# Optimization experiments

Measured on AMD Instinct MI355X. Metric: run time of the kernel, lower is better.

## Reference

```python
import jax, jax.numpy as jnp
import numpy as np

N_HEAD = 16
HEAD_SIZE = 64
N_EMBD = 1024
B, T = 4, 2048
THETA = 10000.0


def _rope_cos_sin(t_len, dim):
    # freqs: (dim//2,), angles: (T, dim//2)
    inv = 1.0 / (THETA ** (jnp.arange(0, dim, 2, dtype=jnp.float32) / dim))
    ang = jnp.arange(t_len, dtype=jnp.float32)[:, None] * inv[None, :]
    return jnp.cos(ang), jnp.sin(ang)


def _apply_rope(x, cos, sin):
    # x: (B, H, T, hs) -> complex-pair rotation over last dim
    xr = x.reshape(*x.shape[:-1], -1, 2)
    x0, x1 = xr[..., 0], xr[..., 1]
    c = cos[None, None, :, :]
    s = sin[None, None, :, :]
    o0 = x0 * c - x1 * s
    o1 = x0 * s + x1 * c
    return jnp.stack([o0, o1], axis=-1).reshape(x.shape)


def setup_inputs() -> dict:
    key = jax.random.key(0)
    ks = jax.random.split(key, 5)
    scale = 1.0 / np.sqrt(N_EMBD)
    return {
        "x": jax.random.normal(ks[0], (B, T, N_EMBD), dtype=jnp.float32),
        "Wq": jax.random.normal(ks[1], (N_EMBD, N_HEAD * HEAD_SIZE), dtype=jnp.float32) * scale,
        "Wk": jax.random.normal(ks[2], (N_EMBD, N_HEAD * HEAD_SIZE), dtype=jnp.float32) * scale,
        "Wv": jax.random.normal(ks[3], (N_EMBD, N_HEAD * HEAD_SIZE), dtype=jnp.float32) * scale,
        "Wp": jax.random.normal(ks[4], (N_HEAD * HEAD_SIZE, N_EMBD), dtype=jnp.float32) * scale,
        "bp": jnp.zeros((N_EMBD,), dtype=jnp.float32),
    }


def reference(x, Wq, Wk, Wv, Wp, bp):
    Bx, Tx, C = x.shape
    q = (x @ Wq).reshape(Bx, Tx, N_HEAD, HEAD_SIZE).transpose(0, 2, 1, 3)
    k = (x @ Wk).reshape(Bx, Tx, N_HEAD, HEAD_SIZE).transpose(0, 2, 1, 3)
    v = (x @ Wv).reshape(Bx, Tx, N_HEAD, HEAD_SIZE).transpose(0, 2, 1, 3)
    cos, sin = _rope_cos_sin(Tx, HEAD_SIZE)
    q = _apply_rope(q, cos, sin)
    k = _apply_rope(k, cos, sin)
    wei = jnp.einsum('bhqd,bhkd->bhqk', q, k) * (HEAD_SIZE ** -0.5)
    causal = jnp.tril(jnp.ones((Tx, Tx), dtype=bool))
    wei = jnp.where(causal[None, None, :, :], wei, -jnp.inf)
    wei = jax.nn.softmax(wei, axis=-1)
    out = jnp.einsum('bhqk,bhkd->bhqd', wei, v)
    out = out.transpose(0, 2, 1, 3).reshape(Bx, Tx, N_HEAD * HEAD_SIZE)
    return out @ Wp + bp
```

## Files before the change

kernel.cpp:

```cpp
#include <hip/hip_runtime.h>
#include <hip/hip_bf16.h>

#define NH 16
#define HS 64
#define CE 1024
#define BB 4
#define TT 2048

typedef __bf16 bf16;
typedef __bf16 v8bf __attribute__((ext_vector_type(8)));
typedef __bf16 v4bf __attribute__((ext_vector_type(4)));
typedef __bf16 v2bf __attribute__((ext_vector_type(2)));
typedef float v4f __attribute__((ext_vector_type(4)));
typedef float v16f __attribute__((ext_vector_type(16)));

#define GLD16(gp, lp)                                                              \
    __builtin_amdgcn_global_load_lds((const __attribute__((address_space(1))) void*)(gp), \
                                     (__attribute__((address_space(3))) void*)(lp), 16, 0, 0)

__global__ __launch_bounds__(256) void cast_x_kernel(const float* __restrict__ x,
                                                     bf16* __restrict__ xb) {
    int idx = (blockIdx.x * 256 + threadIdx.x) * 8;
    const float4* xp = (const float4*)(x + idx);
    float4 a = xp[0], b = xp[1];
    v8bf o;
    o[0] = (bf16)a.x; o[1] = (bf16)a.y; o[2] = (bf16)a.z; o[3] = (bf16)a.w;
    o[4] = (bf16)b.x; o[5] = (bf16)b.y; o[6] = (bf16)b.z; o[7] = (bf16)b.w;
    *(v8bf*)(xb + idx) = o;
}

__global__ __launch_bounds__(256) void transpose_w_kernel(const float* __restrict__ W,
                                                          bf16* __restrict__ Wt) {
    __shared__ bf16 tile[64][66];
    int k0 = blockIdx.x * 64;
    int n0 = blockIdx.y * 64;
    int tx = threadIdx.x & 63;
    int ty = threadIdx.x >> 6;
    for (int s = 0; s < 16; s++) {
        int r = s * 4 + ty;
        tile[r][tx] = (bf16)W[(size_t)(k0 + r) * CE + n0 + tx];
    }
    __syncthreads();
    for (int s = 0; s < 16; s++) {
        int r = s * 4 + ty;
        Wt[(size_t)(n0 + r) * CE + k0 + tx] = tile[tx][r];
    }
}

template <int MODE>
__global__ __launch_bounds__(256) void gemm_bt(const bf16* __restrict__ A,
                                               const bf16* __restrict__ Bt,
                                               void* __restrict__ outp,
                                               const float* __restrict__ bias) {
    __shared__ __align__(16) bf16 As[128 * 32];
    __shared__ __align__(16) bf16 Bs[128 * 32];
    const int tid = threadIdx.x;
    const int lane = tid & 63, wave = tid >> 6;
    const int lane15 = lane & 15, quad = lane >> 4;
    const int wr = wave >> 1, wc = wave & 1;
    const int m0 = blockIdx.y * 128;
    const int n0 = blockIdx.x * 128;

    v4f acc[4][4] = {};

    const int cm = tid >> 2;
    const int ck = (tid & 3) * 8;
    const bf16* Ag = A + (size_t)(m0 + cm) * CE + ck;
    const bf16* Bg = Bt + (size_t)(n0 + cm) * CE + ck;
    bf16* aDst0 = &As[wave * 512];
    bf16* aDst1 = &As[2048 + wave * 512];
    bf16* bDst0 = &Bs[wave * 512];
    bf16* bDst1 = &Bs[2048 + wave * 512];

    for (int k0 = 0; k0 < CE; k0 += 32) {
        __syncthreads();
        GLD16(Ag + k0, aDst0);
        GLD16(Ag + k0 + (size_t)64 * CE, aDst1);
        GLD16(Bg + k0, bDst0);
        GLD16(Bg + k0 + (size_t)64 * CE, bDst1);
        __syncthreads();
        v8bf af[4], bfr[4];
        for (int i = 0; i < 4; i++)
            af[i] = *(const v8bf*)(&As[(wr * 64 + i * 16 + lane15) * 32 + quad * 8]);
        for (int j = 0; j < 4; j++)
            bfr[j] = *(const v8bf*)(&Bs[(wc * 64 + j * 16 + lane15) * 32 + quad * 8]);
        for (int i = 0; i < 4; i++)
            for (int j = 0; j < 4; j++)
                acc[i][j] = __builtin_amdgcn_mfma_f32_16x16x32_bf16(af[i], bfr[j], acc[i][j], 0, 0, 0);
    }

    for (int i = 0; i < 4; i++) {
        for (int j = 0; j < 4; j++) {
            int gmb = m0 + wr * 64 + i * 16 + quad * 4;
            int gn = n0 + wc * 64 + j * 16 + lane15;
            if (MODE == 1) {
                float bb = bias[gn];
                float* out = (float*)outp;
                for (int r = 0; r < 4; r++)
                    out[(size_t)(gmb + r) * CE + gn] = acc[i][j][r] + bb;
            } else if (MODE == 0) {
                bf16* out = (bf16*)outp;
                int h = gn >> 6, d = gn & 63;
                for (int r = 0; r < 4; r++) {
                    int gm = gmb + r;
                    int b = gm >> 11, t = gm & 2047;
                    out[(((size_t)(b * NH + h)) * TT + t) * HS + d] = (bf16)acc[i][j][r];
                }
            } else {
                bf16* out = (bf16*)outp;
                int h = gn >> 6, d = gn & 63;
                int b = gmb >> 11, t = gmb & 2047;
                v4bf pack;
                for (int r = 0; r < 4; r++) pack[r] = (bf16)acc[i][j][r];
                *(v4bf*)(&out[(((size_t)(b * NH + h)) * HS + d) * TT + t]) = pack;
            }
        }
    }
}

__global__ __launch_bounds__(256) void rope_kernel(bf16* __restrict__ Qb, bf16* __restrict__ Kb) {
    unsigned idx = blockIdx.x * 256 + threadIdx.x;
    bf16* buf = blockIdx.y ? Kb : Qb;
    int i = idx & 31;
    int t = (idx >> 5) & 2047;
    float inv = exp2f(-0.41524101186092034f * (float)i);
    float ang = (float)t * inv;
    float s, c;
    sincosf(ang, &s, &c);
    bf16* p = buf + (size_t)idx * 2;
    v2bf v = *(v2bf*)p;
    float x0 = (float)v[0], x1 = (float)v[1];
    v2bf o;
    o[0] = (bf16)(x0 * c - x1 * s);
    o[1] = (bf16)(x0 * s + x1 * c);
    *(v2bf*)p = o;
}

__global__ __launch_bounds__(256, 4) void attn_kernel(const bf16* __restrict__ Qb,
                                                      const bf16* __restrict__ Kb,
                                                      const bf16* __restrict__ Vt,
                                                      bf16* __restrict__ Ob) {
    __shared__ __align__(16) bf16 Ks[32 * 64];
    __shared__ __align__(16) bf16 Vs[64 * 32];
    const int tid = threadIdx.x, lane = tid & 63, wave = tid >> 6;
    const int lane31 = lane & 31, h = lane >> 5;
    const int qb = 15 - (int)(blockIdx.x >> 6);
    const int bh = blockIdx.x & 63;
    const int q0 = qb * 128 + wave * 32;
    const bf16* Qp = Qb + (size_t)bh * TT * HS;
    const bf16* Kp = Kb + (size_t)bh * TT * HS;
    const bf16* Vp = Vt + (size_t)bh * HS * TT;

    v8bf qf[4];
    for (int m = 0; m < 4; m++)
        qf[m] = *(const v8bf*)(Qp + (q0 + lane31) * HS + m * 16 + h * 8);

    v16f o0 = {}, o1 = {};
    float m_i = -3.0e38f, l_i = 0.f;

    const int kr = tid >> 3, kc = tid & 7;
    const bf16* kg = Kp + kr * HS + ((kc ^ (kr & 7)) * 8);
    const int vd = tid >> 2, vc = tid & 3;
    const bf16* vg = Vp + (size_t)vd * TT + ((vc ^ (vd & 3)) * 8);
    bf16* ksDst = &Ks[wave * 512];
    bf16* vsDst = &Vs[wave * 512];

    const float SC = 0.125f;
    const int kv_max = qb * 128 + 96;
    for (int kv0 = 0; kv0 <= kv_max; kv0 += 32) {
        __syncthreads();
        GLD16(kg + kv0 * HS, ksDst);
        GLD16(vg + kv0, vsDst);
        __syncthreads();
        if (kv0 > q0) continue;
        const bool diag = (kv0 == q0);

        v16f s = {};
        for (int m = 0; m < 4; m++) {
            v8bf af = *(const v8bf*)(&Ks[lane31 * 64 + (((m << 1) | h) ^ (lane31 & 7)) * 8]);
            s = __builtin_amdgcn_mfma_f32_32x32x16_bf16(af, qf[m], s, 0, 0, 0);
        }

        float p[16];
        for (int r = 0; r < 16; r++) {
            float v = s[r] * SC;
            if (diag) {
                int kvr = (r & 3) + 8 * (r >> 2) + 4 * h;
                v = (kvr <= lane31) ? v : -3.0e38f;
            }
            p[r] = v;
        }
        float t8[8];
        for (int r = 0; r < 8; r++) t8[r] = fmaxf(p[r], p[r + 8]);
        float t4a = fmaxf(fmaxf(t8[0], t8[1]), fmaxf(t8[2], t8[3]));
        float t4b = fmaxf(fmaxf(t8[4], t8[5]), fmaxf(t8[6], t8[7]));
        float mx = fmaxf(t4a, t4b);
        mx = fmaxf(mx, __shfl_xor(mx, 32));
        float mn = fmaxf(m_i, mx);
        float alpha = __expf(m_i - mn);
        m_i = mn;
        for (int r = 0; r < 16; r++) p[r] = __expf(p[r] - mn);
        float a8[8];
        for (int r = 0; r < 8; r++) a8[r] = p[r] + p[r + 8];
        float s4a = (a8[0] + a8[1]) + (a8[2] + a8[3]);
        float s4b = (a8[4] + a8[5]) + (a8[6] + a8[7]);
        float rs = s4a + s4b;
        rs += __shfl_xor(rs, 32);
        l_i = l_i * alpha + rs;
        for (int r = 0; r < 16; r++) { o0[r] *= alpha; o1[r] *= alpha; }

        union { v4bf v; unsigned long long u; } ch[4];
        for (int g = 0; g < 4; g++)
            for (int rr = 0; rr < 4; rr++)
                ch[g].v[rr] = (bf16)p[g * 4 + rr];

        for (int t = 0; t < 2; t++) {
            unsigned long long mine0 = ch[2 * t].u, mine1 = ch[2 * t + 1].u;
            unsigned long long send = h ? mine0 : mine1;
            unsigned long long recv = __shfl_xor(send, 32);
            union { v8bf v; unsigned long long u[2]; } bfr;
            bfr.u[0] = h ? recv : mine0;
            bfr.u[1] = h ? mine1 : recv;
            int cidx = (((t << 1) | h) ^ (lane31 & 3)) * 8;
            v8bf va0 = *(const v8bf*)(&Vs[lane31 * 32 + cidx]);
            o0 = __builtin_amdgcn_mfma_f32_32x32x16_bf16(va0, bfr.v, o0, 0, 0, 0);
            v8bf va1 = *(const v8bf*)(&Vs[(32 + lane31) * 32 + cidx]);
            o1 = __builtin_amdgcn_mfma_f32_32x32x16_bf16(va1, bfr.v, o1, 0, 0, 0);
        }
    }

    const int b = bh >> 4, hh = bh & 15;
    const int q = q0 + lane31;
    float invl = 1.f / l_i;
    bf16* outRow = Ob + ((size_t)(b * TT + q)) * CE + hh * HS;
    for (int g = 0; g < 4; g++) {
        v4bf w0, w1;
        for (int rr = 0; rr < 4; rr++) {
            w0[rr] = (bf16)(o0[g * 4 + rr] * invl);
            w1[rr] = (bf16)(o1[g * 4 + rr] * invl);
        }
        *(v4bf*)(outRow + g * 8 + h * 4) = w0;
        *(v4bf*)(outRow + 32 + g * 8 + h * 4) = w1;
    }
}

extern "C" void kernel_launch(void* const* d_in, const int* in_sizes, int n_in,
                              void* d_out, int out_size, void* d_ws, size_t ws_size,
                              hipStream_t stream) {
    const float* x  = (const float*)d_in[0];
    const float* Wq = (const float*)d_in[1];
    const float* Wk = (const float*)d_in[2];
    const float* Wv = (const float*)d_in[3];
    const float* Wp = (const float*)d_in[4];
    const float* bp = (const float*)d_in[5];
    char* ws = (char*)d_ws;
    const size_t MB = 1024 * 1024;
    bf16* Xb  = (bf16*)(ws);
    bf16* WqT = (bf16*)(ws + 16 * MB);
    bf16* WkT = (bf16*)(ws + 18 * MB);
    bf16* WvT = (bf16*)(ws + 20 * MB);
    bf16* WpT = (bf16*)(ws + 22 * MB);
    bf16* Qb  = (bf16*)(ws + 24 * MB);
    bf16* Kb  = (bf16*)(ws + 40 * MB);
    bf16* Vt  = (bf16*)(ws + 56 * MB);
    bf16* Ob  = (bf16*)(ws + 72 * MB);

    cast_x_kernel<<<dim3(4096), dim3(256), 0, stream>>>(x, Xb);
    transpose_w_kernel<<<dim3(16, 16), dim3(256), 0, stream>>>(Wq, WqT);
    transpose_w_kernel<<<dim3(16, 16), dim3(256), 0, stream>>>(Wk, WkT);
    transpose_w_kernel<<<dim3(16, 16), dim3(256), 0, stream>>>(Wv, WvT);
    transpose_w_kernel<<<dim3(16, 16), dim3(256), 0, stream>>>(Wp, WpT);

    dim3 gg(8, 64);
    gemm_bt<0><<<gg, dim3(256), 0, stream>>>(Xb, WqT, (void*)Qb, nullptr);
    gemm_bt<0><<<gg, dim3(256), 0, stream>>>(Xb, WkT, (void*)Kb, nullptr);
    gemm_bt<2><<<gg, dim3(256), 0, stream>>>(Xb, WvT, (void*)Vt, nullptr);

    rope_kernel<<<dim3(16384, 2), dim3(256), 0, stream>>>(Qb, Kb);

    attn_kernel<<<dim3(1024), dim3(256), 0, stream>>>(Qb, Kb, Vt, Ob);

    gemm_bt<1><<<gg, dim3(256), 0, stream>>>(Ob, WpT, d_out, bp);
}
```

Measured before the change: 310.0 us.

## Fuse QKV GEMMs, batch weight transposes, pair causal query blocks in attention

Merges the four weight-transpose launches into one grid and the three Q/K/V projections into a single GEMM over a concatenated weight, routing outputs by column range. The GEMM K-tile doubles to 64 to halve the number of barriers. Attention now processes a light and a heavy causal query block per workgroup to balance work, and hoists K/V fragments into registers shared by both. It also folds the softmax scale into Q during RoPE and skips the rescale when no row max changes. The cost is higher register pressure, hence occupancy drops to 2 blocks, and larger shared memory in the GEMM.

After: 302.4 us. 1.03x faster.

```diff
diff --git a/kernel.cpp b/kernel.cpp
--- a/kernel.cpp
+++ b/kernel.cpp
@@ -29,9 +29,16 @@
     *(v8bf*)(xb + idx) = o;
 }
 
-__global__ __launch_bounds__(256) void transpose_w_kernel(const float* __restrict__ W,
-                                                          bf16* __restrict__ Wt) {
+__global__ __launch_bounds__(256) void transpose_w_kernel(const float* __restrict__ W0,
+                                                          const float* __restrict__ W1,
+                                                          const float* __restrict__ W2,
+                                                          const float* __restrict__ W3,
+                                                          bf16* __restrict__ dqkv,
+                                                          bf16* __restrict__ dp) {
     __shared__ bf16 tile[64][66];
+    int z = blockIdx.z;
+    const float* W = (z == 0) ? W0 : (z == 1) ? W1 : (z == 2) ? W2 : W3;
+    bf16* Wt = (z < 3) ? (dqkv + (size_t)z * 1024 * CE) : dp;
     int k0 = blockIdx.x * 64;
     int n0 = blockIdx.y * 64;
     int tx = threadIdx.x & 63;
@@ -50,10 +57,12 @@
 template <int MODE>
 __global__ __launch_bounds__(256) void gemm_bt(const bf16* __restrict__ A,
                                                const bf16* __restrict__ Bt,
-                                               void* __restrict__ outp,
+                                               bf16* __restrict__ Qb_, bf16* __restrict__ Kb_,
+                                               bf16* __restrict__ Vt_,
+                                               float* __restrict__ Pout,
                                                const float* __restrict__ bias) {
-    __shared__ __align__(16) bf16 As[128 * 32];
-    __shared__ __align__(16) bf16 Bs[128 * 32];
+    __shared__ __align__(16) bf16 As[128 * 64];
+    __shared__ __align__(16) bf16 Bs[128 * 64];
     const int tid = threadIdx.x;
     const int lane = tid & 63, wave = tid >> 6;
     const int lane15 = lane & 15, quad = lane >> 4;
@@ -63,30 +72,31 @@
 
     v4f acc[4][4] = {};
 
-    const int cm = tid >> 2;
-    const int ck = (tid & 3) * 8;
+    const int cm = tid >> 3;
+    const int ck = (tid & 7) * 8;
     const bf16* Ag = A + (size_t)(m0 + cm) * CE + ck;
     const bf16* Bg = Bt + (size_t)(n0 + cm) * CE + ck;
-    bf16* aDst0 = &As[wave * 512];
-    bf16* aDst1 = &As[2048 + wave * 512];
-    bf16* bDst0 = &Bs[wave * 512];
-    bf16* bDst1 = &Bs[2048 + wave * 512];
-
-    for (int k0 = 0; k0 < CE; k0 += 32) {
-        __syncthreads();
-        GLD16(Ag + k0, aDst0);
-        GLD16(Ag + k0 + (size_t)64 * CE, aDst1);
-        GLD16(Bg + k0, bDst0);
-        GLD16(Bg + k0 + (size_t)64 * CE, bDst1);
-        __syncthreads();
-        v8bf af[4], bfr[4];
-        for (int i = 0; i < 4; i++)
-            af[i] = *(const v8bf*)(&As[(wr * 64 + i * 16 + lane15) * 32 + quad * 8]);
-        for (int j = 0; j < 4; j++)
-            bfr[j] = *(const v8bf*)(&Bs[(wc * 64 + j * 16 + lane15) * 32 + quad * 8]);
-        for (int i = 0; i < 4; i++)
+    bf16* aD = &As[wave * 512];
+    bf16* bD = &Bs[wave * 512];
+
+    for (int k0 = 0; k0 < CE; k0 += 64) {
+        __syncthreads();
+#pragma unroll
+        for (int p = 0; p < 4; p++) GLD16(Ag + k0 + (size_t)(p * 32) * CE, aD + p * 2048);
+#pragma unroll
+        for (int p = 0; p < 4; p++) GLD16(Bg + k0 + (size_t)(p * 32) * CE, bD + p * 2048);
+        __syncthreads();
+#pragma unroll
+        for (int kh = 0; kh < 2; kh++) {
+            v8bf af[4], bfr[4];
+            for (int i = 0; i < 4; i++)
+                af[i] = *(const v8bf*)(&As[(wr * 64 + i * 16 + lane15) * 64 + kh * 32 + quad * 8]);
             for (int j = 0; j < 4; j++)
-                acc[i][j] = __builtin_amdgcn_mfma_f32_16x16x32_bf16(af[i], bfr[j], acc[i][j], 0, 0, 0);
+                bfr[j] = *(const v8bf*)(&Bs[(wc * 64 + j * 16 + lane15) * 64 + kh * 32 + quad * 8]);
+            for (int i = 0; i < 4; i++)
+                for (int j = 0; j < 4; j++)
+                    acc[i][j] = __builtin_amdgcn_mfma_f32_16x16x32_bf16(af[i], bfr[j], acc[i][j], 0, 0, 0);
+        }
     }
 
     for (int i = 0; i < 4; i++) {
@@ -95,24 +105,25 @@
             int gn = n0 + wc * 64 + j * 16 + lane15;
             if (MODE == 1) {
                 float bb = bias[gn];
-                float* out = (float*)outp;
                 for (int r = 0; r < 4; r++)
-                    out[(size_t)(gmb + r) * CE + gn] = acc[i][j][r] + bb;
-            } else if (MODE == 0) {
-                bf16* out = (bf16*)outp;
-                int h = gn >> 6, d = gn & 63;
-                for (int r = 0; r < 4; r++) {
-                    int gm = gmb + r;
-                    int b = gm >> 11, t = gm & 2047;
-                    out[(((size_t)(b * NH + h)) * TT + t) * HS + d] = (bf16)acc[i][j][r];
+                    Pout[(size_t)(gmb + r) * CE + gn] = acc[i][j][r] + bb;
+            } else {
+                int w = gn >> 10;
+                int n = gn & 1023;
+                int h = n >> 6, d = n & 63;
+                if (w < 2) {
+                    bf16* out = w ? Kb_ : Qb_;
+                    for (int r = 0; r < 4; r++) {
+                        int gm = gmb + r;
+                        int b = gm >> 11, t = gm & 2047;
+                        out[(((size_t)(b * NH + h)) * TT + t) * HS + d] = (bf16)acc[i][j][r];
+                    }
+                } else {
+                    int b = gmb >> 11, t = gmb & 2047;
+                    v4bf pack;
+                    for (int r = 0; r < 4; r++) pack[r] = (bf16)acc[i][j][r];
+                    *(v4bf*)(&Vt_[(((size_t)(b * NH + h)) * HS + d) * TT + t]) = pack;
                 }
-            } else {
-                bf16* out = (bf16*)outp;
-                int h = gn >> 6, d = gn & 63;
-                int b = gmb >> 11, t = gmb & 2047;
-                v4bf pack;
-                for (int r = 0; r < 4; r++) pack[r] = (bf16)acc[i][j][r];
-                *(v4bf*)(&out[(((size_t)(b * NH + h)) * HS + d) * TT + t]) = pack;
             }
         }
     }
@@ -120,13 +131,15 @@
 
 __global__ __launch_bounds__(256) void rope_kernel(bf16* __restrict__ Qb, bf16* __restrict__ Kb) {
     unsigned idx = blockIdx.x * 256 + threadIdx.x;
-    bf16* buf = blockIdx.y ? Kb : Qb;
+    bool isK = blockIdx.y != 0;
+    bf16* buf = isK ? Kb : Qb;
     int i = idx & 31;
     int t = (idx >> 5) & 2047;
     float inv = exp2f(-0.41524101186092034f * (float)i);
     float ang = (float)t * inv;
     float s, c;
     sincosf(ang, &s, &c);
+    if (!isK) { s *= 0.125f; c *= 0.125f; }
     bf16* p = buf + (size_t)idx * 2;
     v2bf v = *(v2bf*)p;
     float x0 = (float)v[0], x1 = (float)v[1];
@@ -136,7 +149,7 @@
     *(v2bf*)p = o;
 }
 
-__global__ __launch_bounds__(256, 4) void attn_kernel(const bf16* __restrict__ Qb,
+__global__ __launch_bounds__(256, 2) void attn_kernel(const bf16* __restrict__ Qb,
                                                       const bf16* __restrict__ Kb,
                                                       const bf16* __restrict__ Vt,
                                                       bf16* __restrict__ Ob) {
@@ -144,19 +157,22 @@
     __shared__ __align__(16) bf16 Vs[64 * 32];
     const int tid = threadIdx.x, lane = tid & 63, wave = tid >> 6;
     const int lane31 = lane & 31, h = lane >> 5;
-    const int qb = 15 - (int)(blockIdx.x >> 6);
+    const int pair = blockIdx.x >> 6;
     const int bh = blockIdx.x & 63;
-    const int q0 = qb * 128 + wave * 32;
+    const int q0A = pair * 128 + wave * 32;
+    const int q0B = (15 - pair) * 128 + wave * 32;
     const bf16* Qp = Qb + (size_t)bh * TT * HS;
     const bf16* Kp = Kb + (size_t)bh * TT * HS;
     const bf16* Vp = Vt + (size_t)bh * HS * TT;
 
-    v8bf qf[4];
-    for (int m = 0; m < 4; m++)
-        qf[m] = *(const v8bf*)(Qp + (q0 + lane31) * HS + m * 16 + h * 8);
-
-    v16f o0 = {}, o1 = {};
-    float m_i = -3.0e38f, l_i = 0.f;
+    v8bf qfA[4], qfB[4];
+    for (int m = 0; m < 4; m++) {
+        qfA[m] = *(const v8bf*)(Qp + (q0A + lane31) * HS + m * 16 + h * 8);
+        qfB[m] = *(const v8bf*)(Qp + (q0B + lane31) * HS + m * 16 + h * 8);
+    }
+
+    v16f oA0 = {}, oA1 = {}, oB0 = {}, oB1 = {};
+    float mA = -3.0e38f, lA = 0.f, mB = -3.0e38f, lB = 0.f;
 
     const int kr = tid >> 3, kc = tid & 7;
     const bf16* kg = Kp + kr * HS + ((kc ^ (kr & 7)) * 8);
@@ -165,25 +181,15 @@
     bf16* ksDst = &Ks[wave * 512];
     bf16* vsDst = &Vs[wave * 512];
 
-    const float SC = 0.125f;
-    const int kv_max = qb * 128 + 96;
-    for (int kv0 = 0; kv0 <= kv_max; kv0 += 32) {
-        __syncthreads();
-        GLD16(kg + kv0 * HS, ksDst);
-        GLD16(vg + kv0, vsDst);
-        __syncthreads();
-        if (kv0 > q0) continue;
-        const bool diag = (kv0 == q0);
-
+    v8bf kf[4], vf[2][2];
+
+    auto step = [&](const v8bf* qf, v16f& o0, v16f& o1, float& m_i, float& l_i, bool diag) {
         v16f s = {};
-        for (int m = 0; m < 4; m++) {
-            v8bf af = *(const v8bf*)(&Ks[lane31 * 64 + (((m << 1) | h) ^ (lane31 & 7)) * 8]);
-            s = __builtin_amdgcn_mfma_f32_32x32x16_bf16(af, qf[m], s, 0, 0, 0);
-        }
-
+        for (int m = 0; m < 4; m++)
+            s = __builtin_amdgcn_mfma_f32_32x32x16_bf16(kf[m], qf[m], s, 0, 0, 0);
         float p[16];
         for (int r = 0; r < 16; r++) {
-            float v = s[r] * SC;
+            float v = s[r];
             if (diag) {
                 int kvr = (r & 3) + 8 * (r >> 2) + 4 * h;
                 v = (kvr <= lane31) ? v : -3.0e38f;
@@ -192,28 +198,28 @@
         }
         float t8[8];
         for (int r = 0; r < 8; r++) t8[r] = fmaxf(p[r], p[r + 8]);
-        float t4a = fmaxf(fmaxf(t8[0], t8[1]), fmaxf(t8[2], t8[3]));
-        float t4b = fmaxf(fmaxf(t8[4], t8[5]), fmaxf(t8[6], t8[7]));
-        float mx = fmaxf(t4a, t4b);
+        float mx = fmaxf(fmaxf(fmaxf(t8[0], t8[1]), fmaxf(t8[2], t8[3])),
+                         fmaxf(fmaxf(t8[4], t8[5]), fmaxf(t8[6], t8[7])));
         mx = fmaxf(mx, __shfl_xor(mx, 32));
+        bool anyUpd = __ballot(mx > m_i) != 0ull;
         float mn = fmaxf(m_i, mx);
-        float alpha = __expf(m_i - mn);
-        m_i = mn;
         for (int r = 0; r < 16; r++) p[r] = __expf(p[r] - mn);
         float a8[8];
         for (int r = 0; r < 8; r++) a8[r] = p[r] + p[r + 8];
-        float s4a = (a8[0] + a8[1]) + (a8[2] + a8[3]);
-        float s4b = (a8[4] + a8[5]) + (a8[6] + a8[7]);
-        float rs = s4a + s4b;
+        float rs = ((a8[0] + a8[1]) + (a8[2] + a8[3])) + ((a8[4] + a8[5]) + (a8[6] + a8[7]));
         rs += __shfl_xor(rs, 32);
-        l_i = l_i * alpha + rs;
-        for (int r = 0; r < 16; r++) { o0[r] *= alpha; o1[r] *= alpha; }
-
+        if (anyUpd) {
+            float alpha = __expf(m_i - mn);
+            m_i = mn;
+            l_i = l_i * alpha + rs;
+            for (int r = 0; r < 16; r++) { o0[r] *= alpha; o1[r] *= alpha; }
+        } else {
+            l_i += rs;
+        }
         union { v4bf v; unsigned long long u; } ch[4];
         for (int g = 0; g < 4; g++)
             for (int rr = 0; rr < 4; rr++)
                 ch[g].v[rr] = (bf16)p[g * 4 + rr];
-
         for (int t = 0; t < 2; t++) {
             unsigned long long mine0 = ch[2 * t].u, mine1 = ch[2 * t + 1].u;
             unsigned long long send = h ? mine0 : mine1;
@@ -221,27 +227,43 @@
             union { v8bf v; unsigned long long u[2]; } bfr;
             bfr.u[0] = h ? recv : mine0;
             bfr.u[1] = h ? mine1 : recv;
-            int cidx = (((t << 1) | h) ^ (lane31 & 3)) * 8;
-            v8bf va0 = *(const v8bf*)(&Vs[lane31 * 32 + cidx]);
-            o0 = __builtin_amdgcn_mfma_f32_32x32x16_bf16(va0, bfr.v, o0, 0, 0, 0);
-            v8bf va1 = *(const v8bf*)(&Vs[(32 + lane31) * 32 + cidx]);
-            o1 = __builtin_amdgcn_mfma_f32_32x32x16_bf16(va1, bfr.v, o1, 0, 0, 0);
-        }
+            o0 = __builtin_amdgcn_mfma_f32_32x32x16_bf16(vf[t][0], bfr.v, o0, 0, 0, 0);
+            o1 = __builtin_amdgcn_mfma_f32_32x32x16_bf16(vf[t][1], bfr.v, o1, 0, 0, 0);
+        }
+    };
+
+    const int kv_end = (15 - pair) * 128 + 96;
+    for (int kv0 = 0; kv0 <= kv_end; kv0 += 32) {
+        __syncthreads();
+        GLD16(kg + kv0 * HS, ksDst);
+        GLD16(vg + kv0, vsDst);
+        __syncthreads();
+        for (int m = 0; m < 4; m++)
+            kf[m] = *(const v8bf*)(&Ks[lane31 * 64 + (((m << 1) | h) ^ (lane31 & 7)) * 8]);
+        for (int t = 0; t < 2; t++)
+            for (int dh = 0; dh < 2; dh++)
+                vf[t][dh] = *(const v8bf*)(&Vs[(dh * 32 + lane31) * 32 + ((((t << 1) | h) ^ (lane31 & 3)) * 8)]);
+        if (kv0 <= q0B) step(qfB, oB0, oB1, mB, lB, kv0 == q0B);
+        if (kv0 <= q0A) step(qfA, oA0, oA1, mA, lA, kv0 == q0A);
     }
 
     const int b = bh >> 4, hh = bh & 15;
-    const int q = q0 + lane31;
-    float invl = 1.f / l_i;
-    bf16* outRow = Ob + ((size_t)(b * TT + q)) * CE + hh * HS;
-    for (int g = 0; g < 4; g++) {
-        v4bf w0, w1;
-        for (int rr = 0; rr < 4; rr++) {
-            w0[rr] = (bf16)(o0[g * 4 + rr] * invl);
-            w1[rr] = (bf16)(o1[g * 4 + rr] * invl);
-        }
-        *(v4bf*)(outRow + g * 8 + h * 4) = w0;
-        *(v4bf*)(outRow + 32 + g * 8 + h * 4) = w1;
-    }
+    auto writeO = [&](int q0, v16f& o0, v16f& o1, float l_i) {
+        int q = q0 + lane31;
+        float invl = 1.f / l_i;
+        bf16* outRow = Ob + ((size_t)(b * TT + q)) * CE + hh * HS;
+        for (int g = 0; g < 4; g++) {
+            v4bf w0, w1;
+            for (int rr = 0; rr < 4; rr++) {
+                w0[rr] = (bf16)(o0[g * 4 + rr] * invl);
+                w1[rr] = (bf16)(o1[g * 4 + rr] * invl);
+            }
+            *(v4bf*)(outRow + g * 8 + h * 4) = w0;
+            *(v4bf*)(outRow + 32 + g * 8 + h * 4) = w1;
+        }
+    };
+    writeO(q0A, oA0, oA1, lA);
+    writeO(q0B, oB0, oB1, lB);
 }
 
 extern "C" void kernel_launch(void* const* d_in, const int* in_sizes, int n_in,
@@ -255,30 +277,23 @@
     const float* bp = (const float*)d_in[5];
     char* ws = (char*)d_ws;
     const size_t MB = 1024 * 1024;
-    bf16* Xb  = (bf16*)(ws);
-    bf16* WqT = (bf16*)(ws + 16 * MB);
-    bf16* WkT = (bf16*)(ws + 18 * MB);
-    bf16* WvT = (bf16*)(ws + 20 * MB);
-    bf16* WpT = (bf16*)(ws + 22 * MB);
-    bf16* Qb  = (bf16*)(ws + 24 * MB);
-    bf16* Kb  = (bf16*)(ws + 40 * MB);
-    bf16* Vt  = (bf16*)(ws + 56 * MB);
-    bf16* Ob  = (bf16*)(ws + 72 * MB);
+    bf16* Xb    = (bf16*)(ws);
+    bf16* WqkvT = (bf16*)(ws + 16 * MB);
+    bf16* WpT   = (bf16*)(ws + 22 * MB);
+    bf16* Qb    = (bf16*)(ws + 24 * MB);
+    bf16* Kb    = (bf16*)(ws + 40 * MB);
+    bf16* Vt    = (bf16*)(ws + 56 * MB);
+    bf16* Ob    = (bf16*)(ws + 72 * MB);
 
     cast_x_kernel<<<dim3(4096), dim3(256), 0, stream>>>(x, Xb);
-    transpose_w_kernel<<<dim3(16, 16), dim3(256), 0, stream>>>(Wq, WqT);
-    transpose_w_kernel<<<dim3(16, 16), dim3(256), 0, stream>>>(Wk, WkT);
-    transpose_w_kernel<<<dim3(16, 16), dim3(256), 0, stream>>>(Wv, WvT);
-    transpose_w_kernel<<<dim3(16, 16), dim3(256), 0, stream>>>(Wp, WpT);
-
-    dim3 gg(8, 64);
-    gemm_bt<0><<<gg, dim3(256), 0, stream>>>(Xb, WqT, (void*)Qb, nullptr);
-    gemm_bt<0><<<gg, dim3(256), 0, stream>>>(Xb, WkT, (void*)Kb, nullptr);
-    gemm_bt<2><<<gg, dim3(256), 0, stream>>>(Xb, WvT, (void*)Vt, nullptr);
+    transpose_w_kernel<<<dim3(16, 16, 4), dim3(256), 0, stream>>>(Wq, Wk, Wv, Wp, WqkvT, WpT);
+
+    gemm_bt<0><<<dim3(24, 64), dim3(256), 0, stream>>>(Xb, WqkvT, Qb, Kb, Vt, nullptr, nullptr);
 
     rope_kernel<<<dim3(16384, 2), dim3(256), 0, stream>>>(Qb, Kb);
 
-    attn_kernel<<<dim3(1024), dim3(256), 0, stream>>>(Qb, Kb, Vt, Ob);
-
-    gemm_bt<1><<<gg, dim3(256), 0, stream>>>(Ob, WpT, d_out, bp);
-}
+    attn_kernel<<<dim3(512), dim3(256), 0, stream>>>(Qb, Kb, Vt, Ob);
+
+    gemm_bt<1><<<dim3(8, 64), dim3(256), 0, stream>>>(Ob, WpT, nullptr, nullptr, nullptr,
+                                                      (float*)d_out, bp);
+}
```
